# Optimization experiments

Hardware: AMD Instinct MI355X
Metric: run time of the kernel (lower is better)

Reference implementation:

```python
import jax, jax.numpy as jnp
import numpy as np

C = 256
H_HEADS = 8
HEAD_DIM = C // H_HEADS
B, H, W = 2, 64, 64


def conv1x1(x, w, b):
    # x: [B,C,H,W], w: [O,C], b: [O]
    return jnp.einsum('oc,bchw->bohw', w, x) + b[None, :, None, None]


def setup_inputs() -> dict:
    key = jax.random.key(0)
    ks = jax.random.split(key, 12)
    s = 1.0 / np.sqrt(C)
    inp = {
        'query': jax.random.normal(ks[0], (B, C, H, W), jnp.float32),
        'key': jax.random.normal(ks[1], (B, C, H, W), jnp.float32),
        'value': jax.random.normal(ks[2], (B, C, H, W), jnp.float32),
        'wq': jax.random.uniform(ks[3], (C, C), jnp.float32, -s, s),
        'bq': jax.random.uniform(ks[4], (C,), jnp.float32, -s, s),
        'wk': jax.random.uniform(ks[5], (C, C), jnp.float32, -s, s),
        'bk': jax.random.uniform(ks[6], (C,), jnp.float32, -s, s),
        'wv': jax.random.uniform(ks[7], (C, C), jnp.float32, -s, s),
        'bv': jax.random.uniform(ks[8], (C,), jnp.float32, -s, s),
        'wo': jax.random.uniform(ks[9], (C, C), jnp.float32, -s, s),
        'bo': jax.random.uniform(ks[10], (C,), jnp.float32, -s, s),
    }
    return inp


def reference(query, key, value, wq, bq, wk, bk, wv, bv, wo, bo):
    b, c, h, w = query.shape
    hw = h * w
    q = conv1x1(query, wq, bq).reshape(b, H_HEADS, HEAD_DIM, hw)  # [B,nh,hd,HW]
    k = conv1x1(key, wk, bk).reshape(b, H_HEADS, HEAD_DIM, hw)
    v = conv1x1(value, wv, bv).reshape(b, H_HEADS, HEAD_DIM, hw)
    # scores: [B,nh,HW,HW]
    scores = jnp.einsum('bhdq,bhdk->bqhk'.replace('q', 'i').replace('k', 'j'), q, k)  # placeholder avoided
    scores = jnp.einsum('bhdi,bhdj->bhij', q, k) / np.sqrt(HEAD_DIM).astype(np.float32)
    attn = jax.nn.softmax(scores, axis=-1)
    out = jnp.einsum('bhij,bhdj->bhdi', attn, v)  # [B,nh,hd,HW]
    out = out.reshape(b, c, h, w)
    return conv1x1(out, wo, bo)
```

## Files before the change

### kernel.cpp

```cpp
#include <hip/hip_runtime.h>
#include <hip/hip_bf16.h>

#define C_DIM 256
#define HW    4096
#define NH    8
#define HD    32

typedef unsigned short u16;
typedef __attribute__((ext_vector_type(8)))  short bf16x8;
typedef __attribute__((ext_vector_type(4)))  float f32x4;
typedef __attribute__((ext_vector_type(16))) float f32x16;

#define QSCALE 0.25503486f

#if __has_builtin(__builtin_amdgcn_exp2f)
#define EXP2(x) __builtin_amdgcn_exp2f(x)
#else
#define EXP2(x) exp2f(x)
#endif

__device__ __forceinline__ u16 f2bf(float x) {
  __hip_bfloat16 h = __float2bfloat16(x);
  return __builtin_bit_cast(u16, h);
}
__device__ __forceinline__ bf16x8 ld8(const u16* p) {
  return *(const bf16x8*)p;
}
__device__ __forceinline__ f32x16 zero16() {
  f32x16 z;
#pragma unroll
  for (int i = 0; i < 16; ++i) z[i] = 0.0f;
  return z;
}

__device__ __forceinline__ unsigned cvtpk(float lo, float hi) {
  unsigned r;
  asm("v_cvt_pk_bf16_f32 %0, %1, %2" : "=v"(r) : "v"(lo), "v"(hi));
  return r;
}

__device__ __forceinline__ void permswap(unsigned& a, unsigned& b) {
#if __has_builtin(__builtin_amdgcn_permlane32_swap)
  auto r = __builtin_amdgcn_permlane32_swap(a, b, false, false);
  a = r[0];
  b = r[1];
#else
  asm volatile("s_nop 1\n\tv_permlane32_swap_b32 %0, %1" : "+v"(a), "+v"(b));
#endif
}

__global__ __launch_bounds__(256) void cast_kernel(
    const float* __restrict__ xq, const float* __restrict__ xk, const float* __restrict__ xv,
    const float* __restrict__ wq, const float* __restrict__ wk,
    const float* __restrict__ wv, const float* __restrict__ wo,
    u16* __restrict__ xT, u16* __restrict__ Wbf) {
  const int z = blockIdx.z;
  const int tx = threadIdx.x, ty = threadIdx.y;
  if (z == 6) {
    int gid = (blockIdx.y * 128 + blockIdx.x) * 256 + ty * 32 + tx;
    int wi = gid >> 16, e = gid & 65535;
    const float* s = (wi == 0) ? wq : (wi == 1) ? wk : (wi == 2) ? wv : wo;
    Wbf[gid] = f2bf(s[e]);
    return;
  }
  __shared__ float lds[32][33];
  const int t = z >> 1, b = z & 1;
  const float* src = (t == 0) ? xq : (t == 1) ? xk : xv;
  const int p0 = blockIdx.x * 32, c0 = blockIdx.y * 32;
#pragma unroll
  for (int j = 0; j < 4; ++j) {
    int c = c0 + ty + j * 8;
    lds[ty + j * 8][tx] = src[(b * C_DIM + c) * HW + p0 + tx];
  }
  __syncthreads();
  u16* dst = xT + (t * 2 + b) * (HW * C_DIM);
#pragma unroll
  for (int j = 0; j < 4; ++j) {
    int p = p0 + ty + j * 8;
    dst[p * C_DIM + c0 + tx] = f2bf(lds[tx][ty + j * 8]);
  }
}

__global__ __launch_bounds__(256) void gemm_qkv_kernel(
    const u16* __restrict__ xT, const u16* __restrict__ Wbf,
    const float* __restrict__ bq, const float* __restrict__ bk,
    const float* __restrict__ bvb,
    u16* __restrict__ qws, u16* __restrict__ kws, u16* __restrict__ vtws) {
  const int lane = threadIdx.x & 63;
  const int wave = threadIdx.x >> 6;
  const int l15 = lane & 15, l4 = lane >> 4;
  const int z = blockIdx.z;
  if (z < 4) {
    const int which = z >> 1, b = z & 1;
    const int m0 = blockIdx.x * 64 + (wave >> 1) * 32;
    const int n0 = blockIdx.y * 64 + (wave & 1) * 32;
    const u16* A  = xT + (which * 2 + b) * (HW * C_DIM);
    const u16* Bw = Wbf + which * (C_DIM * C_DIM);
    f32x4 acc[2][2] = {};
#pragma unroll
    for (int k0 = 0; k0 < 256; k0 += 32) {
      bf16x8 a0 = ld8(A + (m0 + l15) * 256 + k0 + l4 * 8);
      bf16x8 a1 = ld8(A + (m0 + 16 + l15) * 256 + k0 + l4 * 8);
      bf16x8 b0 = ld8(Bw + (n0 + l15) * 256 + k0 + l4 * 8);
      bf16x8 b1 = ld8(Bw + (n0 + 16 + l15) * 256 + k0 + l4 * 8);
      acc[0][0] = __builtin_amdgcn_mfma_f32_16x16x32_bf16(a0, b0, acc[0][0], 0, 0, 0);
      acc[0][1] = __builtin_amdgcn_mfma_f32_16x16x32_bf16(a0, b1, acc[0][1], 0, 0, 0);
      acc[1][0] = __builtin_amdgcn_mfma_f32_16x16x32_bf16(a1, b0, acc[1][0], 0, 0, 0);
      acc[1][1] = __builtin_amdgcn_mfma_f32_16x16x32_bf16(a1, b1, acc[1][1], 0, 0, 0);
    }
    const float scale = (which == 0) ? QSCALE : 1.0f;
    const float* bias = (which == 0) ? bq : bk;
    u16* out = (which == 0) ? qws : kws;
#pragma unroll
    for (int nt = 0; nt < 2; ++nt) {
      int o = n0 + nt * 16 + l15;
      int hh = o >> 5, d = o & 31;
      float bv = bias[o];
#pragma unroll
      for (int mt = 0; mt < 2; ++mt) {
#pragma unroll
        for (int r = 0; r < 4; ++r) {
          int p = m0 + mt * 16 + l4 * 4 + r;
          out[((b * NH + hh) * HW + p) * HD + d] = f2bf((acc[mt][nt][r] + bv) * scale);
        }
      }
    }
  } else {
    const int b = z - 4;
    const int m0 = blockIdx.y * 64 + (wave >> 1) * 32;
    const int n0 = blockIdx.x * 64 + (wave & 1) * 32;
    const u16* A  = Wbf + 2 * (C_DIM * C_DIM);
    const u16* Bx = xT + (2 * 2 + b) * (HW * C_DIM);
    f32x4 acc[2][2] = {};
#pragma unroll
    for (int k0 = 0; k0 < 256; k0 += 32) {
      bf16x8 a0 = ld8(A + (m0 + l15) * 256 + k0 + l4 * 8);
      bf16x8 a1 = ld8(A + (m0 + 16 + l15) * 256 + k0 + l4 * 8);
      bf16x8 b0 = ld8(Bx + (n0 + l15) * 256 + k0 + l4 * 8);
      bf16x8 b1 = ld8(Bx + (n0 + 16 + l15) * 256 + k0 + l4 * 8);
      acc[0][0] = __builtin_amdgcn_mfma_f32_16x16x32_bf16(a0, b0, acc[0][0], 0, 0, 0);
      acc[0][1] = __builtin_amdgcn_mfma_f32_16x16x32_bf16(a0, b1, acc[0][1], 0, 0, 0);
      acc[1][0] = __builtin_amdgcn_mfma_f32_16x16x32_bf16(a1, b0, acc[1][0], 0, 0, 0);
      acc[1][1] = __builtin_amdgcn_mfma_f32_16x16x32_bf16(a1, b1, acc[1][1], 0, 0, 0);
    }
#pragma unroll
    for (int mt = 0; mt < 2; ++mt) {
#pragma unroll
      for (int r = 0; r < 4; ++r) {
        int o = m0 + mt * 16 + l4 * 4 + r;
        float bvv = bvb[o];
#pragma unroll
        for (int nt = 0; nt < 2; ++nt) {
          int p = n0 + nt * 16 + l15;
          vtws[(b * C_DIM + o) * HW + p] = f2bf(acc[mt][nt][r] + bvv);
        }
      }
    }
  }
}

__device__ __forceinline__ void tile_step(const f32x16& st, bf16x8 va0, bf16x8 va1,
                                          f32x16& acc, float& lsum) {
  float p[16];
#pragma unroll
  for (int r = 0; r < 16; ++r) p[r] = EXP2(st[r]);
  float s0 = (p[0] + p[1]) + (p[2] + p[3]);
  float s1 = (p[4] + p[5]) + (p[6] + p[7]);
  float s2 = (p[8] + p[9]) + (p[10] + p[11]);
  float s3 = (p[12] + p[13]) + (p[14] + p[15]);
  lsum += (s0 + s1) + (s2 + s3);
  unsigned pk[8];
#pragma unroll
  for (int rr = 0; rr < 8; ++rr) pk[rr] = cvtpk(p[2 * rr], p[2 * rr + 1]);
  permswap(pk[0], pk[2]);
  permswap(pk[1], pk[3]);
  permswap(pk[4], pk[6]);
  permswap(pk[5], pk[7]);
  union { unsigned u[4]; bf16x8 v; } pb0, pb1;
  pb0.u[0] = pk[0]; pb0.u[1] = pk[1]; pb0.u[2] = pk[2]; pb0.u[3] = pk[3];
  pb1.u[0] = pk[4]; pb1.u[1] = pk[5]; pb1.u[2] = pk[6]; pb1.u[3] = pk[7];
  __builtin_amdgcn_s_setprio(1);
  acc = __builtin_amdgcn_mfma_f32_32x32x16_bf16(va0, pb0.v, acc, 0, 0, 0);
  acc = __builtin_amdgcn_mfma_f32_32x32x16_bf16(va1, pb1.v, acc, 0, 0, 0);
  __builtin_amdgcn_s_setprio(0);
}

__global__ __launch_bounds__(256, 4) void attn_kernel(
    const u16* __restrict__ qws, const u16* __restrict__ kws,
    const u16* __restrict__ vtws, u16* __restrict__ attno) {
  const int lane = threadIdx.x & 63;
  const int sp = threadIdx.x >> 6;
  const int l5 = lane & 31, h5 = lane >> 5;
  const int bh = blockIdx.x;
  const int b = bh >> 3, h = bh & 7;
  const int q0 = blockIdx.y * 64;
  const u16* qb = qws + bh * (HW * HD);
  const u16* kb = kws + bh * (HW * HD);
  const u16* vb = vtws + (b * C_DIM + h * HD + l5) * HW;

  bf16x8 qA0 = ld8(qb + (q0 + l5) * HD + h5 * 8);
  bf16x8 qA1 = ld8(qb + (q0 + l5) * HD + 16 + h5 * 8);
  bf16x8 qB0 = ld8(qb + (q0 + 32 + l5) * HD + h5 * 8);
  bf16x8 qB1 = ld8(qb + (q0 + 32 + l5) * HD + 16 + h5 * 8);
  f32x16 accA = zero16(), accB = zero16();
  const f32x16 zv = zero16();
  float lsA = 0.0f, lsB = 0.0f;

  const int j_beg = sp * (HW / 4), j_end = j_beg + (HW / 4);
  bf16x8 kf0 = ld8(kb + (j_beg + l5) * HD + h5 * 8);
  bf16x8 kf1 = ld8(kb + (j_beg + l5) * HD + 16 + h5 * 8);
  for (int j0 = j_beg; j0 < j_end; j0 += 32) {
    bf16x8 va0 = ld8(vb + j0 + h5 * 8);
    bf16x8 va1 = ld8(vb + j0 + 16 + h5 * 8);
    f32x16 st = __builtin_amdgcn_mfma_f32_32x32x16_bf16(kf0, qA0, zv, 0, 0, 0);
    st = __builtin_amdgcn_mfma_f32_32x32x16_bf16(kf1, qA1, st, 0, 0, 0);
    f32x16 st2 = __builtin_amdgcn_mfma_f32_32x32x16_bf16(kf0, qB0, zv, 0, 0, 0);
    st2 = __builtin_amdgcn_mfma_f32_32x32x16_bf16(kf1, qB1, st2, 0, 0, 0);
    const int jn = (j0 + 32 < j_end) ? j0 + 32 : j_beg;
    kf0 = ld8(kb + (jn + l5) * HD + h5 * 8);
    kf1 = ld8(kb + (jn + l5) * HD + 16 + h5 * 8);
    tile_step(st, va0, va1, accA, lsA);
    tile_step(st2, va0, va1, accB, lsB);
  }

  __shared__ float redA[3][2][1024];
  __shared__ float redL[3][2][64];
  if (sp != 0) {
#pragma unroll
    for (int r = 0; r < 16; ++r) {
      int d = (r & 3) + 8 * (r >> 2) + 4 * h5;
      redA[sp - 1][0][d * 32 + l5] = accA[r];
      redA[sp - 1][1][d * 32 + l5] = accB[r];
    }
    redL[sp - 1][0][h5 * 32 + l5] = lsA;
    redL[sp - 1][1][h5 * 32 + l5] = lsB;
  }
  __syncthreads();
  if (sp == 0) {
#pragma unroll
    for (int r = 0; r < 16; ++r) {
      int d = (r & 3) + 8 * (r >> 2) + 4 * h5;
      accA[r] += (redA[0][0][d * 32 + l5] + redA[1][0][d * 32 + l5]) +
                 redA[2][0][d * 32 + l5];
      accB[r] += (redA[0][1][d * 32 + l5] + redA[1][1][d * 32 + l5]) +
                 redA[2][1][d * 32 + l5];
    }
    lsA += (redL[0][0][h5 * 32 + l5] + redL[1][0][h5 * 32 + l5]) +
           redL[2][0][h5 * 32 + l5];
    lsB += (redL[0][1][h5 * 32 + l5] + redL[1][1][h5 * 32 + l5]) +
           redL[2][1][h5 * 32 + l5];
    unsigned uaA = __builtin_bit_cast(unsigned, lsA), ubA = uaA;
    permswap(uaA, ubA);
    float totA = __builtin_bit_cast(float, uaA) + __builtin_bit_cast(float, ubA);
    unsigned uaB = __builtin_bit_cast(unsigned, lsB), ubB = uaB;
    permswap(uaB, ubB);
    float totB = __builtin_bit_cast(float, uaB) + __builtin_bit_cast(float, ubB);
    const float invA = 1.0f / totA, invB = 1.0f / totB;
    u16* obA = attno + (bh * HW + q0 + l5) * HD;
    u16* obB = attno + (bh * HW + q0 + 32 + l5) * HD;
#pragma unroll
    for (int r = 0; r < 16; ++r) {
      int d = (r & 3) + 8 * (r >> 2) + 4 * h5;
      obA[d] = f2bf(accA[r] * invA);
      obB[d] = f2bf(accB[r] * invB);
    }
  }
}

__global__ __launch_bounds__(256) void gemm_o_kernel(
    const u16* __restrict__ attno, const u16* __restrict__ Wbf,
    const float* __restrict__ bo, float* __restrict__ outp) {
  const int lane = threadIdx.x & 63;
  const int wave = threadIdx.x >> 6;
  const int l15 = lane & 15, l4 = lane >> 4;
  const int b = blockIdx.z;
  const int m0 = blockIdx.y * 64 + (wave >> 1) * 32;
  const int n0 = blockIdx.x * 64 + (wave & 1) * 32;
  const u16* A  = Wbf + 3 * (C_DIM * C_DIM);
  const u16* Bx = attno + b * (NH * HW * HD);
  f32x4 acc[2][2] = {};
#pragma unroll
  for (int k0 = 0; k0 < 256; k0 += 32) {
    int ks = k0 >> 5;
    bf16x8 a0 = ld8(A + (m0 + l15) * 256 + k0 + l4 * 8);
    bf16x8 a1 = ld8(A + (m0 + 16 + l15) * 256 + k0 + l4 * 8);
    bf16x8 b0 = ld8(Bx + (ks * HW + n0 + l15) * HD + l4 * 8);
    bf16x8 b1 = ld8(Bx + (ks * HW + n0 + 16 + l15) * HD + l4 * 8);
    acc[0][0] = __builtin_amdgcn_mfma_f32_16x16x32_bf16(a0, b0, acc[0][0], 0, 0, 0);
    acc[0][1] = __builtin_amdgcn_mfma_f32_16x16x32_bf16(a0, b1, acc[0][1], 0, 0, 0);
    acc[1][0] = __builtin_amdgcn_mfma_f32_16x16x32_bf16(a1, b0, acc[1][0], 0, 0, 0);
    acc[1][1] = __builtin_amdgcn_mfma_f32_16x16x32_bf16(a1, b1, acc[1][1], 0, 0, 0);
  }
#pragma unroll
  for (int mt = 0; mt < 2; ++mt) {
#pragma unroll
    for (int r = 0; r < 4; ++r) {
      int o = m0 + mt * 16 + l4 * 4 + r;
      float bvv = bo[o];
#pragma unroll
      for (int nt = 0; nt < 2; ++nt) {
        int p = n0 + nt * 16 + l15;
        outp[(b * C_DIM + o) * HW + p] = acc[mt][nt][r] + bvv;
      }
    }
  }
}

extern "C" void kernel_launch(void* const* d_in, const int* in_sizes, int n_in,
                              void* d_out, int out_size, void* d_ws, size_t ws_size,
                              hipStream_t stream) {
  const float* xq = (const float*)d_in[0];
  const float* xk = (const float*)d_in[1];
  const float* xv = (const float*)d_in[2];
  const float* wq = (const float*)d_in[3];
  const float* bq = (const float*)d_in[4];
  const float* wk = (const float*)d_in[5];
  const float* bk = (const float*)d_in[6];
  const float* wv = (const float*)d_in[7];
  const float* bv = (const float*)d_in[8];
  const float* wo = (const float*)d_in[9];
  const float* bo = (const float*)d_in[10];

  if (ws_size < 29884416u) return;
  char* ws = (char*)d_ws;
  u16* xT    = (u16*)(ws);
  u16* Wbf   = (u16*)(ws + 12582912);
  u16* qws   = (u16*)(ws + 13107200);
  u16* kws   = (u16*)(ws + 17301504);
  u16* vtws  = (u16*)(ws + 21495808);
  u16* attno = (u16*)(ws + 25690112);

  cast_kernel<<<dim3(128, 8, 7), dim3(32, 8), 0, stream>>>(xq, xk, xv, wq, wk, wv, wo, xT, Wbf);
  gemm_qkv_kernel<<<dim3(64, 4, 6), dim3(256), 0, stream>>>(xT, Wbf, bq, bk, bv, qws, kws, vtws);
  attn_kernel<<<dim3(16, 64), dim3(256), 0, stream>>>(qws, kws, vtws, attno);
  gemm_o_kernel<<<dim3(64, 4, 2), dim3(256), 0, stream>>>(attno, Wbf, bo, (float*)d_out);
}
```

Baseline: 109.9 us.

## Stream K tiles through LDS with direct global-to-LDS double-buffered loads

```diff
diff --git a/kernel.cpp b/kernel.cpp
--- a/kernel.cpp
+++ b/kernel.cpp
@@ -31,6 +31,12 @@
 #pragma unroll
   for (int i = 0; i < 16; ++i) z[i] = 0.0f;
   return z;
+}
+
+__device__ __forceinline__ void g2lds(const u16* g, u16* l) {
+  __builtin_amdgcn_global_load_lds(
+      (const __attribute__((address_space(1))) unsigned int*)g,
+      (__attribute__((address_space(3))) unsigned int*)l, 16, 0, 0);
 }
 
 __device__ __forceinline__ unsigned cvtpk(float lo, float hi) {
@@ -198,6 +204,11 @@
   const u16* kb = kws + bh * (HW * HD);
   const u16* vb = vtws + (b * C_DIM + h * HD + l5) * HW;
 
+  __shared__ __align__(16) char arena[26112];
+  u16* stK = (u16*)arena + sp * 2048;
+  const u16* ldsrd = stK + lane * 8;
+  const u16* ksrc = kb + (lane & 31) * HD + (lane >> 5) * 8;
+
   bf16x8 qA0 = ld8(qb + (q0 + l5) * HD + h5 * 8);
   bf16x8 qA1 = ld8(qb + (q0 + l5) * HD + 16 + h5 * 8);
   bf16x8 qB0 = ld8(qb + (q0 + 32 + l5) * HD + h5 * 8);
@@ -207,48 +218,70 @@
   float lsA = 0.0f, lsB = 0.0f;
 
   const int j_beg = sp * (HW / 4), j_end = j_beg + (HW / 4);
-  bf16x8 kf0 = ld8(kb + (j_beg + l5) * HD + h5 * 8);
-  bf16x8 kf1 = ld8(kb + (j_beg + l5) * HD + 16 + h5 * 8);
-  for (int j0 = j_beg; j0 < j_end; j0 += 32) {
-    bf16x8 va0 = ld8(vb + j0 + h5 * 8);
-    bf16x8 va1 = ld8(vb + j0 + 16 + h5 * 8);
-    f32x16 st = __builtin_amdgcn_mfma_f32_32x32x16_bf16(kf0, qA0, zv, 0, 0, 0);
-    st = __builtin_amdgcn_mfma_f32_32x32x16_bf16(kf1, qA1, st, 0, 0, 0);
-    f32x16 st2 = __builtin_amdgcn_mfma_f32_32x32x16_bf16(kf0, qB0, zv, 0, 0, 0);
-    st2 = __builtin_amdgcn_mfma_f32_32x32x16_bf16(kf1, qB1, st2, 0, 0, 0);
-    const int jn = (j0 + 32 < j_end) ? j0 + 32 : j_beg;
-    kf0 = ld8(kb + (jn + l5) * HD + h5 * 8);
-    kf1 = ld8(kb + (jn + l5) * HD + 16 + h5 * 8);
-    tile_step(st, va0, va1, accA, lsA);
-    tile_step(st2, va0, va1, accB, lsB);
-  }
-
-  __shared__ float redA[3][2][1024];
-  __shared__ float redL[3][2][64];
+  g2lds(ksrc + j_beg * HD,      stK);
+  g2lds(ksrc + j_beg * HD + 16, stK + 512);
+
+  for (int j0 = j_beg; j0 < j_end; j0 += 64) {
+    {
+      bf16x8 va0 = ld8(vb + j0 + h5 * 8);
+      bf16x8 va1 = ld8(vb + j0 + 16 + h5 * 8);
+      g2lds(ksrc + (j0 + 32) * HD,      stK + 1024);
+      g2lds(ksrc + (j0 + 32) * HD + 16, stK + 1536);
+      asm volatile("s_waitcnt vmcnt(4)" ::: "memory");
+      bf16x8 kf0 = ld8(ldsrd);
+      bf16x8 kf1 = ld8(ldsrd + 512);
+      f32x16 st = __builtin_amdgcn_mfma_f32_32x32x16_bf16(kf0, qA0, zv, 0, 0, 0);
+      st = __builtin_amdgcn_mfma_f32_32x32x16_bf16(kf1, qA1, st, 0, 0, 0);
+      tile_step(st, va0, va1, accA, lsA);
+      f32x16 st2 = __builtin_amdgcn_mfma_f32_32x32x16_bf16(kf0, qB0, zv, 0, 0, 0);
+      st2 = __builtin_amdgcn_mfma_f32_32x32x16_bf16(kf1, qB1, st2, 0, 0, 0);
+      tile_step(st2, va0, va1, accB, lsB);
+    }
+    {
+      const int jn = (j0 + 64 < j_end) ? j0 + 64 : j_beg;
+      bf16x8 va0 = ld8(vb + j0 + 32 + h5 * 8);
+      bf16x8 va1 = ld8(vb + j0 + 48 + h5 * 8);
+      g2lds(ksrc + jn * HD,      stK);
+      g2lds(ksrc + jn * HD + 16, stK + 512);
+      asm volatile("s_waitcnt vmcnt(4)" ::: "memory");
+      bf16x8 kf0 = ld8(ldsrd + 1024);
+      bf16x8 kf1 = ld8(ldsrd + 1536);
+      f32x16 st = __builtin_amdgcn_mfma_f32_32x32x16_bf16(kf0, qA0, zv, 0, 0, 0);
+      st = __builtin_amdgcn_mfma_f32_32x32x16_bf16(kf1, qA1, st, 0, 0, 0);
+      tile_step(st, va0, va1, accA, lsA);
+      f32x16 st2 = __builtin_amdgcn_mfma_f32_32x32x16_bf16(kf0, qB0, zv, 0, 0, 0);
+      st2 = __builtin_amdgcn_mfma_f32_32x32x16_bf16(kf1, qB1, st2, 0, 0, 0);
+      tile_step(st2, va0, va1, accB, lsB);
+    }
+  }
+
+  float* redA = (float*)arena;
+  float* redL = (float*)(arena + 24576);
+  __syncthreads();
   if (sp != 0) {
 #pragma unroll
     for (int r = 0; r < 16; ++r) {
       int d = (r & 3) + 8 * (r >> 2) + 4 * h5;
-      redA[sp - 1][0][d * 32 + l5] = accA[r];
-      redA[sp - 1][1][d * 32 + l5] = accB[r];
-    }
-    redL[sp - 1][0][h5 * 32 + l5] = lsA;
-    redL[sp - 1][1][h5 * 32 + l5] = lsB;
+      redA[((sp - 1) * 2 + 0) * 1024 + d * 32 + l5] = accA[r];
+      redA[((sp - 1) * 2 + 1) * 1024 + d * 32 + l5] = accB[r];
+    }
+    redL[((sp - 1) * 2 + 0) * 64 + h5 * 32 + l5] = lsA;
+    redL[((sp - 1) * 2 + 1) * 64 + h5 * 32 + l5] = lsB;
   }
   __syncthreads();
   if (sp == 0) {
 #pragma unroll
     for (int r = 0; r < 16; ++r) {
       int d = (r & 3) + 8 * (r >> 2) + 4 * h5;
-      accA[r] += (redA[0][0][d * 32 + l5] + redA[1][0][d * 32 + l5]) +
-                 redA[2][0][d * 32 + l5];
-      accB[r] += (redA[0][1][d * 32 + l5] + redA[1][1][d * 32 + l5]) +
-                 redA[2][1][d * 32 + l5];
-    }
-    lsA += (redL[0][0][h5 * 32 + l5] + redL[1][0][h5 * 32 + l5]) +
-           redL[2][0][h5 * 32 + l5];
-    lsB += (redL[0][1][h5 * 32 + l5] + redL[1][1][h5 * 32 + l5]) +
-           redL[2][1][h5 * 32 + l5];
+      accA[r] += (redA[0 * 1024 + d * 32 + l5] + redA[2 * 1024 + d * 32 + l5]) +
+                 redA[4 * 1024 + d * 32 + l5];
+      accB[r] += (redA[1 * 1024 + d * 32 + l5] + redA[3 * 1024 + d * 32 + l5]) +
+                 redA[5 * 1024 + d * 32 + l5];
+    }
+    lsA += (redL[0 * 64 + h5 * 32 + l5] + redL[2 * 64 + h5 * 32 + l5]) +
+           redL[4 * 64 + h5 * 32 + l5];
+    lsB += (redL[1 * 64 + h5 * 32 + l5] + redL[3 * 64 + h5 * 32 + l5]) +
+           redL[5 * 64 + h5 * 32 + l5];
     unsigned uaA = __builtin_bit_cast(unsigned, lsA), ubA = uaA;
     permswap(uaA, ubA);
     float totA = __builtin_bit_cast(float, uaA) + __builtin_bit_cast(float, ubA);
```

New measurement: 238.3 us. +116.9%, slower.
